# Kernel optimization log

Measured on AMD Instinct MI355X. Metric: run time of the kernel, lower is better.

Reference implementation:

```python
import jax, jax.numpy as jnp
import numpy as np

K = 121          # kernel_size
C = 3            # channels
PAD = (K - 1) // 2  # 60, replicate padding so output matches input spatial size


def setup_inputs() -> dict:
    key = jax.random.key(0)
    k1, k2 = jax.random.split(key)
    x = jax.random.normal(k1, (8, C, 512, 512), dtype=jnp.float32)
    sigma = jax.random.uniform(k2, (), dtype=jnp.float32)
    return {"x": x, "sigma": sigma}


def _gaussian_kernel(sigma):
    # sigma -> sigma*8 + 16, variance = sigma**2 (as in torch forward)
    s = sigma * 8.0 + 16.0
    variance = s * s
    coord = jnp.arange(K, dtype=jnp.float32) - (K - 1) / 2.0  # centered coords
    diff = -(coord[:, None] ** 2 + coord[None, :] ** 2)       # [K,K], -((x-m)^2+(y-m)^2)
    kern = jnp.exp(diff / (2.0 * variance))
    # the 1/(2*pi*variance) prefactor cancels under normalization
    kern = kern / jnp.sum(kern)
    return kern


def reference(x, sigma):
    kern = _gaussian_kernel(sigma)
    # depthwise weights: [out_ch=C, in_ch/groups=1, K, K]
    w = jnp.broadcast_to(kern[None, None, :, :], (C, 1, K, K))
    # replicate padding (torch 'replicate' == jnp 'edge')
    xp = jnp.pad(x, ((0, 0), (0, 0), (PAD, PAD), (PAD, PAD)), mode="edge")
    out = jax.lax.conv_general_dilated(
        xp, w,
        window_strides=(1, 1),
        padding="VALID",
        dimension_numbers=("NCHW", "OIHW", "NCHW"),
        feature_group_count=C,
    )
    return out
```

## Files before the change

### kernel.cpp

```cpp
#include <hip/hip_runtime.h>


#define HH    512
#define WW    512
#define NIMG  24
#define RAD   60
#define KTAPS 128

__global__ void gauss_weights(const float* __restrict__ sigma,
                              float* __restrict__ wgt) {
    const int i = threadIdx.x;
    const float s = sigma[0] * 8.0f + 16.0f;
    const float inv2v = 1.0f / (2.0f * s * s);
    float g = 0.0f;
    if (i < 121) {
        const float c = (float)i - 60.0f;
        g = expf(-(c * c) * inv2v);
    }
    __shared__ float red[128];
    red[i] = g;
    __syncthreads();
    for (int off = 64; off > 0; off >>= 1) {
        if (i < off) red[i] += red[i + off];
        __syncthreads();
    }
    wgt[i] = g / red[0];
}

#define V_TW     32
#define V_TH     256
#define V_INROWS 384

#define INNER8(CUR, NXT, KO)                                              \
    _Pragma("unroll")                                                     \
    for (int ki = 0; ki < 8; ++ki) {                                      \
        NXT[ki] = sm4[(r0 + ((KO) + 1) * 8 + ki) * 8 + tx];               \
        const float wk = wgt[(KO) * 8 + ki];                              \
        _Pragma("unroll")                                                 \
        for (int j = 0; j < 8; ++j) {                                     \
            const int idx = ki + j;                                       \
            const float4 v = (idx < 8) ? CUR[idx] : NXT[idx - 8];         \
            acc[j].x += wk * v.x; acc[j].y += wk * v.y;                   \
            acc[j].z += wk * v.z; acc[j].w += wk * v.w;                   \
        }                                                                 \
    }

__global__ __launch_bounds__(256, 3) void blur_v(
        const float* __restrict__ x, const float* __restrict__ wgt,
        float* __restrict__ tmp) {
    __shared__ float sm[V_INROWS * V_TW];
    const int tid = threadIdx.x;
    const int w0  = blockIdx.x * V_TW;
    const int h0  = blockIdx.y * V_TH;
    const float* __restrict__ src = x + (size_t)blockIdx.z * (HH * WW);

    {
        const int fc = (tid & 7) * 4;
        int r = tid >> 3;
        #pragma unroll
        for (int it = 0; it < 12; ++it, r += 32) {
            int gr = h0 - RAD + r;
            gr = gr < 0 ? 0 : (gr > HH - 1 ? HH - 1 : gr);
            *(float4*)&sm[r * V_TW + fc] =
                *(const float4*)&src[(size_t)gr * WW + w0 + fc];
        }
    }
    __syncthreads();

    const int tx = tid & 7;
    const int r0 = (tid >> 3) * 8;
    const float4* __restrict__ sm4 = (const float4*)sm;

    float4 acc[8];
    #pragma unroll
    for (int j = 0; j < 8; ++j) acc[j] = make_float4(0.f, 0.f, 0.f, 0.f);

    float4 wa[8], wb[8];
    #pragma unroll
    for (int m = 0; m < 8; ++m) wa[m] = sm4[(r0 + m) * 8 + tx];

    #pragma unroll 1
    for (int ko = 0; ko < 16; ko += 2) {
        INNER8(wa, wb, ko)
        INNER8(wb, wa, ko + 1)
    }

    float* __restrict__ dst = tmp + (size_t)blockIdx.z * (HH * WW);
    #pragma unroll
    for (int j = 0; j < 8; ++j)
        *(float4*)&dst[(size_t)(h0 + r0 + j) * WW + w0 + tx * 4] = acc[j];
}

#define HP_ROW 960

__global__ __launch_bounds__(256, 4) void blur_h(
        const float* __restrict__ tmp, const float* __restrict__ wgt,
        float* __restrict__ out) {
    __shared__ float sm[4 * HP_ROW];
    const int tid = threadIdx.x;
    const int h0  = blockIdx.x * 4;
    const float* __restrict__ src = tmp + (size_t)blockIdx.y * (HH * WW);

    for (int c = tid; c < 640; c += 256) {
        int gc = c - RAD;
        gc = gc < 0 ? 0 : (gc > WW - 1 ? WW - 1 : gc);
        const int la = ((c >> 3) * 12) + (c & 7);
        #pragma unroll
        for (int r = 0; r < 4; ++r)
            sm[r * HP_ROW + la] = src[(size_t)(h0 + r) * WW + gc];
    }
    __syncthreads();

    const int row  = tid >> 6;
    const int lane = tid & 63;
    const float* __restrict__ bs = sm + row * HP_ROW + lane * 12;

    float accA[4] = {0.f, 0.f, 0.f, 0.f};
    float accB[4] = {0.f, 0.f, 0.f, 0.f};
    #pragma unroll
    for (int s = 0; s < 34; ++s) {
        const float4 v = *(const float4*)(bs + (s >> 1) * 12 + (s & 1) * 4);
        const float va[4] = {v.x, v.y, v.z, v.w};
        #pragma unroll
        for (int cc = 0; cc < 4; ++cc) {
            const int p = 4 * s + cc;
            #pragma unroll
            for (int j = 0; j < 8; ++j) {
                const int k = p - j;
                if (k >= 0 && k < KTAPS) {
                    const float wk = wgt[k];
                    if (j < 4) accA[j]     += wk * va[cc];
                    else       accB[j - 4] += wk * va[cc];
                }
            }
        }
    }

    float* __restrict__ dst = out + (size_t)blockIdx.y * (HH * WW)
                                  + (size_t)(h0 + row) * WW + lane * 8;
    *(float4*)dst       = make_float4(accA[0], accA[1], accA[2], accA[3]);
    *(float4*)(dst + 4) = make_float4(accB[0], accB[1], accB[2], accB[3]);
}

extern "C" void kernel_launch(void* const* d_in, const int* in_sizes, int n_in,
                              void* d_out, int out_size, void* d_ws, size_t ws_size,
                              hipStream_t stream) {
    const float* x     = (const float*)d_in[0];
    const float* sigma = (const float*)d_in[1];
    float* out = (float*)d_out;

    float* wgt = (float*)d_ws;
    float* tmp = (float*)d_ws + 512;

    gauss_weights<<<dim3(1), dim3(128), 0, stream>>>(sigma, wgt);
    blur_v<<<dim3(WW / V_TW, HH / V_TH, NIMG), dim3(256), 0, stream>>>(x, wgt, tmp);
    blur_h<<<dim3(HH / 4, NIMG), dim3(256), 0, stream>>>(tmp, wgt, out);
}
```

Before: 120.0 us.

## Fuse Gaussian weight generation into blur kernels and restructure horizontal pass

Drops the separate single-block weights kernel; each blur block now computes the normalized Gaussian taps itself into LDS using a per-thread serial sum with fast exp. Weights are read from LDS in vector chunks instead of global memory. The horizontal pass is rewritten as a sliding-window register loop over octets with a rolled outer loop, mirroring the vertical pass, instead of a fully unrolled scalar tap loop. This removes one launch and the dependency on a tiny kernel, at the cost of redundant per-block exp work (121 exps per thread) and slightly different weight precision from __expf.

```diff
diff --git a/kernel.cpp b/kernel.cpp
--- a/kernel.cpp
+++ b/kernel.cpp
@@ -1,57 +1,57 @@
 #include <hip/hip_runtime.h>
 
 
-#define HH    512
-#define WW    512
-#define NIMG  24
-#define RAD   60
-#define KTAPS 128
+#define HH   512
+#define WW   512
+#define NIMG 24
+#define RAD  60
 
-__global__ void gauss_weights(const float* __restrict__ sigma,
-                              float* __restrict__ wgt) {
-    const int i = threadIdx.x;
+__device__ __forceinline__ void make_weights(const float* __restrict__ sigma,
+                                             float* __restrict__ wlds, int tid) {
     const float s = sigma[0] * 8.0f + 16.0f;
     const float inv2v = 1.0f / (2.0f * s * s);
-    float g = 0.0f;
-    if (i < 121) {
-        const float c = (float)i - 60.0f;
-        g = expf(-(c * c) * inv2v);
+    float sum = 0.0f;
+    #pragma unroll
+    for (int k = 0; k <= 120; ++k) {
+        const float c = (float)k - 60.0f;
+        sum += __expf(-c * c * inv2v);
     }
-    __shared__ float red[128];
-    red[i] = g;
-    __syncthreads();
-    for (int off = 64; off > 0; off >>= 1) {
-        if (i < off) red[i] += red[i + off];
-        __syncthreads();
+    if (tid < 128) {
+        float g = 0.0f;
+        if (tid < 121) {
+            const float c = (float)tid - 60.0f;
+            g = __expf(-c * c * inv2v);
+        }
+        wlds[tid] = g / sum;
     }
-    wgt[i] = g / red[0];
 }
 
-#define V_TW     32
-#define V_TH     256
-#define V_INROWS 384
 
-#define INNER8(CUR, NXT, KO)                                              \
-    _Pragma("unroll")                                                     \
-    for (int ki = 0; ki < 8; ++ki) {                                      \
-        NXT[ki] = sm4[(r0 + ((KO) + 1) * 8 + ki) * 8 + tx];               \
-        const float wk = wgt[(KO) * 8 + ki];                              \
-        _Pragma("unroll")                                                 \
-        for (int j = 0; j < 8; ++j) {                                     \
-            const int idx = ki + j;                                       \
-            const float4 v = (idx < 8) ? CUR[idx] : NXT[idx - 8];         \
-            acc[j].x += wk * v.x; acc[j].y += wk * v.y;                   \
-            acc[j].z += wk * v.z; acc[j].w += wk * v.w;                   \
-        }                                                                 \
+#define V_OCT(CUR, NXT, KO)                                               \
+    { *(float4*)&wq[0] = *(const float4*)&wlds[(KO) * 8];                 \
+      *(float4*)&wq[4] = *(const float4*)&wlds[(KO) * 8 + 4];             \
+      _Pragma("unroll")                                                   \
+      for (int ki = 0; ki < 8; ++ki) {                                    \
+          NXT[ki] = sm4[(r0 + ((KO) + 1) * 8 + ki) * 8 + tx];             \
+          const float wk = wq[ki];                                        \
+          _Pragma("unroll")                                               \
+          for (int j = 0; j < 8; ++j) {                                   \
+              const int idx = ki + j;                                     \
+              const float4 v = (idx < 8) ? CUR[idx] : NXT[idx - 8];       \
+              acc[j].x += wk * v.x; acc[j].y += wk * v.y;                 \
+              acc[j].z += wk * v.z; acc[j].w += wk * v.w;                 \
+          }                                                               \
+      }                                                                   \
     }
 
 __global__ __launch_bounds__(256, 3) void blur_v(
-        const float* __restrict__ x, const float* __restrict__ wgt,
+        const float* __restrict__ x, const float* __restrict__ sigma,
         float* __restrict__ tmp) {
-    __shared__ float sm[V_INROWS * V_TW];
+    __shared__ float sm[384 * 32];
+    __shared__ float wlds[128];
     const int tid = threadIdx.x;
-    const int w0  = blockIdx.x * V_TW;
-    const int h0  = blockIdx.y * V_TH;
+    const int w0  = blockIdx.x * 32;
+    const int h0  = blockIdx.y * 256;
     const float* __restrict__ src = x + (size_t)blockIdx.z * (HH * WW);
 
     {
@@ -61,10 +61,11 @@
         for (int it = 0; it < 12; ++it, r += 32) {
             int gr = h0 - RAD + r;
             gr = gr < 0 ? 0 : (gr > HH - 1 ? HH - 1 : gr);
-            *(float4*)&sm[r * V_TW + fc] =
+            *(float4*)&sm[r * 32 + fc] =
                 *(const float4*)&src[(size_t)gr * WW + w0 + fc];
         }
     }
+    make_weights(sigma, wlds, tid);
     __syncthreads();
 
     const int tx = tid & 7;
@@ -76,13 +77,14 @@
     for (int j = 0; j < 8; ++j) acc[j] = make_float4(0.f, 0.f, 0.f, 0.f);
 
     float4 wa[8], wb[8];
+    float  wq[8];
     #pragma unroll
     for (int m = 0; m < 8; ++m) wa[m] = sm4[(r0 + m) * 8 + tx];
 
     #pragma unroll 1
     for (int ko = 0; ko < 16; ko += 2) {
-        INNER8(wa, wb, ko)
-        INNER8(wb, wa, ko + 1)
+        V_OCT(wa, wb, ko)
+        V_OCT(wb, wa, ko + 1)
     }
 
     float* __restrict__ dst = tmp + (size_t)blockIdx.z * (HH * WW);
@@ -93,53 +95,70 @@
 
 #define HP_ROW 960
 
+#define H_OCT(CUR, NXT, KO)                                               \
+    { const int gbase = (lane + (KO) + 1) * 12;                           \
+      *(float4*)&NXT[0] = *(const float4*)&bs[gbase];                     \
+      *(float4*)&NXT[4] = *(const float4*)&bs[gbase + 4];                 \
+      *(float4*)&wq[0] = *(const float4*)&wlds[(KO) * 8];                 \
+      *(float4*)&wq[4] = *(const float4*)&wlds[(KO) * 8 + 4];             \
+      _Pragma("unroll")                                                   \
+      for (int ki = 0; ki < 8; ++ki) {                                    \
+          const float wk = wq[ki];                                        \
+          _Pragma("unroll")                                               \
+          for (int j = 0; j < 8; ++j) {                                   \
+              const int idx = ki + j;                                     \
+              const float v = (idx < 8) ? CUR[idx] : NXT[idx - 8];        \
+              acc[j] += wk * v;                                           \
+          }                                                               \
+      }                                                                   \
+    }
+
 __global__ __launch_bounds__(256, 4) void blur_h(
-        const float* __restrict__ tmp, const float* __restrict__ wgt,
+        const float* __restrict__ tmp, const float* __restrict__ sigma,
         float* __restrict__ out) {
     __shared__ float sm[4 * HP_ROW];
+    __shared__ float wlds[128];
     const int tid = threadIdx.x;
     const int h0  = blockIdx.x * 4;
     const float* __restrict__ src = tmp + (size_t)blockIdx.y * (HH * WW);
 
-    for (int c = tid; c < 640; c += 256) {
-        int gc = c - RAD;
-        gc = gc < 0 ? 0 : (gc > WW - 1 ? WW - 1 : gc);
-        const int la = ((c >> 3) * 12) + (c & 7);
-        #pragma unroll
-        for (int r = 0; r < 4; ++r)
-            sm[r * HP_ROW + la] = src[(size_t)(h0 + r) * WW + gc];
+    #pragma unroll
+    for (int it = 0; it < 3; ++it) {
+        const int c = tid + it * 256;
+        if (c < 640) {
+            int gc = c - RAD;
+            gc = gc < 0 ? 0 : (gc > WW - 1 ? WW - 1 : gc);
+            const int la = ((c >> 3) * 12) + (c & 7);
+            #pragma unroll
+            for (int r = 0; r < 4; ++r)
+                sm[r * HP_ROW + la] = src[(size_t)(h0 + r) * WW + gc];
+        }
     }
+    make_weights(sigma, wlds, tid);
     __syncthreads();
 
     const int row  = tid >> 6;
     const int lane = tid & 63;
-    const float* __restrict__ bs = sm + row * HP_ROW + lane * 12;
+    const float* __restrict__ bs = sm + row * HP_ROW;
 
-    float accA[4] = {0.f, 0.f, 0.f, 0.f};
-    float accB[4] = {0.f, 0.f, 0.f, 0.f};
+    float a[8], b[8], wq[8];
+    float acc[8];
     #pragma unroll
-    for (int s = 0; s < 34; ++s) {
-        const float4 v = *(const float4*)(bs + (s >> 1) * 12 + (s & 1) * 4);
-        const float va[4] = {v.x, v.y, v.z, v.w};
-        #pragma unroll
-        for (int cc = 0; cc < 4; ++cc) {
-            const int p = 4 * s + cc;
-            #pragma unroll
-            for (int j = 0; j < 8; ++j) {
-                const int k = p - j;
-                if (k >= 0 && k < KTAPS) {
-                    const float wk = wgt[k];
-                    if (j < 4) accA[j]     += wk * va[cc];
-                    else       accB[j - 4] += wk * va[cc];
-                }
-            }
-        }
+    for (int j = 0; j < 8; ++j) acc[j] = 0.0f;
+
+    *(float4*)&a[0] = *(const float4*)&bs[lane * 12];
+    *(float4*)&a[4] = *(const float4*)&bs[lane * 12 + 4];
+
+    #pragma unroll 1
+    for (int ko = 0; ko < 16; ko += 2) {
+        H_OCT(a, b, ko)
+        H_OCT(b, a, ko + 1)
     }
 
     float* __restrict__ dst = out + (size_t)blockIdx.y * (HH * WW)
                                   + (size_t)(h0 + row) * WW + lane * 8;
-    *(float4*)dst       = make_float4(accA[0], accA[1], accA[2], accA[3]);
-    *(float4*)(dst + 4) = make_float4(accB[0], accB[1], accB[2], accB[3]);
+    *(float4*)dst       = make_float4(acc[0], acc[1], acc[2], acc[3]);
+    *(float4*)(dst + 4) = make_float4(acc[4], acc[5], acc[6], acc[7]);
 }
 
 extern "C" void kernel_launch(void* const* d_in, const int* in_sizes, int n_in,
@@ -148,11 +167,8 @@
     const float* x     = (const float*)d_in[0];
     const float* sigma = (const float*)d_in[1];
     float* out = (float*)d_out;
+    float* tmp = (float*)d_ws;
 
-    float* wgt = (float*)d_ws;
-    float* tmp = (float*)d_ws + 512;
-
-    gauss_weights<<<dim3(1), dim3(128), 0, stream>>>(sigma, wgt);
-    blur_v<<<dim3(WW / V_TW, HH / V_TH, NIMG), dim3(256), 0, stream>>>(x, wgt, tmp);
-    blur_h<<<dim3(HH / 4, NIMG), dim3(256), 0, stream>>>(tmp, wgt, out);
+    blur_v<<<dim3(WW / 32, HH / 256, NIMG), dim3(256), 0, stream>>>(x, sigma, tmp);
+    blur_h<<<dim3(HH / 4, NIMG), dim3(256), 0, stream>>>(tmp, sigma, out);
 }
```

Result: slower. 125.0 us (+4.2%).

## Replace separable blur passes with one transposing vertical kernel run twice

Applied to the files above, without the earlier changes.

Replaces the LDS-tiled vertical pass and the separate horizontal pass with a single vertical-blur kernel that reads global memory directly with clamped rows and writes its output transposed. Running it twice (x→tmp, tmp→out) gives the horizontal blur as a vertical blur on transposed data, so the output comes back in the original orientation. Each block also computes the Gaussian weights itself, which removes the separate weight kernel launch. The trade-offs are uncoalesced, strided transposed stores, redundant per-thread computation of the 121-term weight sum, and no LDS reuse of input rows, so the kernel relies on cache hits.

```diff
diff --git a/kernel.cpp b/kernel.cpp
--- a/kernel.cpp
+++ b/kernel.cpp
@@ -1,145 +1,96 @@
 #include <hip/hip_runtime.h>
 
 
+#define WW    512
 #define HH    512
-#define WW    512
+#define PLANE (512 * 512)
 #define NIMG  24
 #define RAD   60
-#define KTAPS 128
 
-__global__ void gauss_weights(const float* __restrict__ sigma,
-                              float* __restrict__ wgt) {
-    const int i = threadIdx.x;
+__device__ __forceinline__ void make_weights(const float* __restrict__ sigma,
+                                             float* __restrict__ wlds, int tid) {
     const float s = sigma[0] * 8.0f + 16.0f;
     const float inv2v = 1.0f / (2.0f * s * s);
-    float g = 0.0f;
-    if (i < 121) {
-        const float c = (float)i - 60.0f;
-        g = expf(-(c * c) * inv2v);
+    float sum = 0.0f;
+    #pragma unroll
+    for (int k = 0; k <= 120; ++k) {
+        const float c = (float)k - 60.0f;
+        sum += __expf(-c * c * inv2v);
     }
-    __shared__ float red[128];
-    red[i] = g;
-    __syncthreads();
-    for (int off = 64; off > 0; off >>= 1) {
-        if (i < off) red[i] += red[i + off];
-        __syncthreads();
+    if (tid < 128) {
+        float g = 0.0f;
+        if (tid < 121) {
+            const float c = (float)tid - 60.0f;
+            g = __expf(-c * c * inv2v);
+        }
+        wlds[tid] = g / sum;
     }
-    wgt[i] = g / red[0];
 }
 
-#define V_TW     32
-#define V_TH     256
-#define V_INROWS 384
-
-#define INNER8(CUR, NXT, KO)                                              \
-    _Pragma("unroll")                                                     \
-    for (int ki = 0; ki < 8; ++ki) {                                      \
-        NXT[ki] = sm4[(r0 + ((KO) + 1) * 8 + ki) * 8 + tx];               \
-        const float wk = wgt[(KO) * 8 + ki];                              \
-        _Pragma("unroll")                                                 \
-        for (int j = 0; j < 8; ++j) {                                     \
-            const int idx = ki + j;                                       \
-            const float4 v = (idx < 8) ? CUR[idx] : NXT[idx - 8];         \
-            acc[j].x += wk * v.x; acc[j].y += wk * v.y;                   \
-            acc[j].z += wk * v.z; acc[j].w += wk * v.w;                   \
-        }                                                                 \
+#define OCT(CUR, NXT, KO)                                                   \
+    { *(float4*)&wq[0] = *(const float4*)&wlds[(KO) * 8];                   \
+      *(float4*)&wq[4] = *(const float4*)&wlds[(KO) * 8 + 4];               \
+      _Pragma("unroll")                                                     \
+      for (int ki = 0; ki < 8; ++ki) {                                      \
+          int rr = r0 - 52 + (KO) * 8 + ki;                                 \
+          rr = rr < 0 ? 0 : (rr > HH - 1 ? HH - 1 : rr);                    \
+          NXT[ki] = *(const float4*)&src[(size_t)rr * WW];                  \
+          const float wk = wq[ki];                                          \
+          _Pragma("unroll")                                                 \
+          for (int j = 0; j < 8; ++j) {                                     \
+              const int idx = ki + j;                                       \
+              const float4 v = (idx < 8) ? CUR[idx] : NXT[idx - 8];         \
+              acc[j].x += wk * v.x; acc[j].y += wk * v.y;                   \
+              acc[j].z += wk * v.z; acc[j].w += wk * v.w;                   \
+          }                                                                 \
+      }                                                                     \
     }
 
-__global__ __launch_bounds__(256, 3) void blur_v(
-        const float* __restrict__ x, const float* __restrict__ wgt,
-        float* __restrict__ tmp) {
-    __shared__ float sm[V_INROWS * V_TW];
-    const int tid = threadIdx.x;
-    const int w0  = blockIdx.x * V_TW;
-    const int h0  = blockIdx.y * V_TH;
-    const float* __restrict__ src = x + (size_t)blockIdx.z * (HH * WW);
+#define STORE_T(CC, COMP)                                                   \
+    { float4 lo = make_float4(acc[0].COMP, acc[1].COMP,                     \
+                              acc[2].COMP, acc[3].COMP);                    \
+      float4 hi = make_float4(acc[4].COMP, acc[5].COMP,                     \
+                              acc[6].COMP, acc[7].COMP);                    \
+      float* p = dst + (size_t)(col + (CC)) * WW + r0;                      \
+      *(float4*)p       = lo;                                               \
+      *(float4*)(p + 4) = hi; }
 
-    {
-        const int fc = (tid & 7) * 4;
-        int r = tid >> 3;
-        #pragma unroll
-        for (int it = 0; it < 12; ++it, r += 32) {
-            int gr = h0 - RAD + r;
-            gr = gr < 0 ? 0 : (gr > HH - 1 ? HH - 1 : gr);
-            *(float4*)&sm[r * V_TW + fc] =
-                *(const float4*)&src[(size_t)gr * WW + w0 + fc];
-        }
+__global__ __launch_bounds__(256, 3) void blur_vt(
+        const float* __restrict__ in, const float* __restrict__ sigma,
+        float* __restrict__ outT) {
+    __shared__ float wlds[128];
+    const int tid  = threadIdx.x;
+    const int quad = tid & 127;
+    const int g8   = tid >> 7;
+    const int col  = quad * 4;
+    const int r0   = blockIdx.x * 16 + g8 * 8;
+    const float* __restrict__ src = in + (size_t)blockIdx.y * PLANE + col;
+
+    float4 wa[8], wb[8], acc[8];
+    float  wq[8];
+
+    #pragma unroll
+    for (int m = 0; m < 8; ++m) {
+        int rr = r0 - 60 + m;
+        rr = rr < 0 ? 0 : rr;
+        wa[m] = *(const float4*)&src[(size_t)rr * WW];
     }
-    __syncthreads();
-
-    const int tx = tid & 7;
-    const int r0 = (tid >> 3) * 8;
-    const float4* __restrict__ sm4 = (const float4*)sm;
-
-    float4 acc[8];
+    make_weights(sigma, wlds, tid);
     #pragma unroll
     for (int j = 0; j < 8; ++j) acc[j] = make_float4(0.f, 0.f, 0.f, 0.f);
-
-    float4 wa[8], wb[8];
-    #pragma unroll
-    for (int m = 0; m < 8; ++m) wa[m] = sm4[(r0 + m) * 8 + tx];
+    __syncthreads();
 
     #pragma unroll 1
     for (int ko = 0; ko < 16; ko += 2) {
-        INNER8(wa, wb, ko)
-        INNER8(wb, wa, ko + 1)
+        OCT(wa, wb, ko)
+        OCT(wb, wa, ko + 1)
     }
 
-    float* __restrict__ dst = tmp + (size_t)blockIdx.z * (HH * WW);
-    #pragma unroll
-    for (int j = 0; j < 8; ++j)
-        *(float4*)&dst[(size_t)(h0 + r0 + j) * WW + w0 + tx * 4] = acc[j];
-}
-
-#define HP_ROW 960
-
-__global__ __launch_bounds__(256, 4) void blur_h(
-        const float* __restrict__ tmp, const float* __restrict__ wgt,
-        float* __restrict__ out) {
-    __shared__ float sm[4 * HP_ROW];
-    const int tid = threadIdx.x;
-    const int h0  = blockIdx.x * 4;
-    const float* __restrict__ src = tmp + (size_t)blockIdx.y * (HH * WW);
-
-    for (int c = tid; c < 640; c += 256) {
-        int gc = c - RAD;
-        gc = gc < 0 ? 0 : (gc > WW - 1 ? WW - 1 : gc);
-        const int la = ((c >> 3) * 12) + (c & 7);
-        #pragma unroll
-        for (int r = 0; r < 4; ++r)
-            sm[r * HP_ROW + la] = src[(size_t)(h0 + r) * WW + gc];
-    }
-    __syncthreads();
-
-    const int row  = tid >> 6;
-    const int lane = tid & 63;
-    const float* __restrict__ bs = sm + row * HP_ROW + lane * 12;
-
-    float accA[4] = {0.f, 0.f, 0.f, 0.f};
-    float accB[4] = {0.f, 0.f, 0.f, 0.f};
-    #pragma unroll
-    for (int s = 0; s < 34; ++s) {
-        const float4 v = *(const float4*)(bs + (s >> 1) * 12 + (s & 1) * 4);
-        const float va[4] = {v.x, v.y, v.z, v.w};
-        #pragma unroll
-        for (int cc = 0; cc < 4; ++cc) {
-            const int p = 4 * s + cc;
-            #pragma unroll
-            for (int j = 0; j < 8; ++j) {
-                const int k = p - j;
-                if (k >= 0 && k < KTAPS) {
-                    const float wk = wgt[k];
-                    if (j < 4) accA[j]     += wk * va[cc];
-                    else       accB[j - 4] += wk * va[cc];
-                }
-            }
-        }
-    }
-
-    float* __restrict__ dst = out + (size_t)blockIdx.y * (HH * WW)
-                                  + (size_t)(h0 + row) * WW + lane * 8;
-    *(float4*)dst       = make_float4(accA[0], accA[1], accA[2], accA[3]);
-    *(float4*)(dst + 4) = make_float4(accB[0], accB[1], accB[2], accB[3]);
+    float* __restrict__ dst = outT + (size_t)blockIdx.y * PLANE;
+    STORE_T(0, x)
+    STORE_T(1, y)
+    STORE_T(2, z)
+    STORE_T(3, w)
 }
 
 extern "C" void kernel_launch(void* const* d_in, const int* in_sizes, int n_in,
@@ -148,11 +99,9 @@
     const float* x     = (const float*)d_in[0];
     const float* sigma = (const float*)d_in[1];
     float* out = (float*)d_out;
+    float* tmp = (float*)d_ws;
 
-    float* wgt = (float*)d_ws;
-    float* tmp = (float*)d_ws + 512;
-
-    gauss_weights<<<dim3(1), dim3(128), 0, stream>>>(sigma, wgt);
-    blur_v<<<dim3(WW / V_TW, HH / V_TH, NIMG), dim3(256), 0, stream>>>(x, wgt, tmp);
-    blur_h<<<dim3(HH / 4, NIMG), dim3(256), 0, stream>>>(tmp, wgt, out);
+    const dim3 grid(HH / 16, NIMG);
+    blur_vt<<<grid, dim3(256), 0, stream>>>(x, sigma, tmp);
+    blur_vt<<<grid, dim3(256), 0, stream>>>(tmp, sigma, out);
 }
```

Result: slower. 148.8 us (+24.0%).
